# Kernel tuning notes

Hardware: AMD Instinct MI355X
Metric: run time of the kernel (lower is better)

The kernel has to match this reference:

```python
import jax, jax.numpy as jnp
import numpy as np

BZ, D_IN, D_STATE, D_OUT, L = 8, 256, 512, 256, 4096


def setup_inputs() -> dict:
    key = jax.random.key(0)
    k_u, k_a, k_b, k_c = jax.random.split(key, 4)
    init_scale = 0.5
    u = jax.random.normal(k_u, (BZ, D_IN, L), dtype=jnp.float32)
    A_unconstrained = jax.random.normal(k_a, (D_STATE,), dtype=jnp.float32) * 0.1
    B_mat = jax.random.normal(k_b, (D_STATE, D_IN), dtype=jnp.float32) * init_scale / np.sqrt(D_IN)
    C_mat = jax.random.normal(k_c, (D_OUT, D_STATE), dtype=jnp.float32) * init_scale / np.sqrt(D_STATE)
    D_mat = jnp.zeros((D_OUT, D_IN), dtype=jnp.float32)
    h0 = jnp.zeros((D_STATE,), dtype=jnp.float32)
    return {"u": u, "A_unconstrained": A_unconstrained, "B_mat": B_mat,
            "C_mat": C_mat, "D_mat": D_mat, "h0": h0}


def reference(u, A_unconstrained, B_mat, C_mat, D_mat, h0):
    # u: (B, input_dim, L)
    Bz = u.shape[0]
    A_diag = -jax.nn.softplus(A_unconstrained)          # (S,)
    # Precompute input projection for all timesteps: (L, B, S)
    Bu = jnp.einsum('bil,si->lbs', u, B_mat)
    state0 = jnp.broadcast_to(h0[None, :], (Bz, A_diag.shape[0]))

    def step(state, bu_t):
        x_t = state * A_diag[None, :] + bu_t            # (B, S)
        return x_t, x_t

    _, xs = jax.lax.scan(step, state0, Bu)              # xs: (L, B, S)
    # y_t = x_t @ C^T + u_t @ D^T, assembled as (B, output_dim, L)
    Y = jnp.einsum('lbs,os->bol', xs, C_mat) + jnp.einsum('bil,oi->bol', u, D_mat)
    return Y
```

## Files before the change

kernel.cpp:

```cpp
#include <hip/hip_runtime.h>
#include <math.h>

#define BZ 8
#define DI 256
#define DS 512
#define DOUT 256
#define LL 4096
#define BS (BZ * DS)
#define CH 64
#define CT 64

typedef __bf16 bf16x8 __attribute__((ext_vector_type(8)));
typedef float f32x4 __attribute__((ext_vector_type(4)));

__device__ __forceinline__ ushort f2b(float f) {
    union { float f; unsigned u; } v; v.f = f;
    unsigned r = v.u + 0x7FFFu + ((v.u >> 16) & 1u);
    return (ushort)(r >> 16);
}
__device__ __forceinline__ float b2f(ushort h) {
    union { unsigned u; float f; } v; v.u = ((unsigned)h) << 16;
    return v.f;
}

__device__ __forceinline__ void gload16(const ushort* g, ushort* l) {
    __builtin_amdgcn_global_load_lds(
        (const __attribute__((address_space(1))) unsigned int*)g,
        (__attribute__((address_space(3))) unsigned int*)l,
        16, 0, 0);
}

__global__ __launch_bounds__(256) void k_prep(const float* __restrict__ Au,
                                              float* __restrict__ apow,
                                              const float* __restrict__ Bm,
                                              const float* __restrict__ Cm,
                                              const float* __restrict__ Dm,
                                              ushort* __restrict__ Bmb,
                                              ushort* __restrict__ Cmb,
                                              ushort* __restrict__ Dmb) {
    const int t = blockIdx.x * 256 + threadIdx.x;
    const int n1 = DS * DI / 4, n2 = DOUT * DS / 4, n3 = DOUT * DI / 4;
    if (t < n1) {
        float4 v = ((const float4*)Bm)[t];
        ushort4 o; o.x = f2b(v.x); o.y = f2b(v.y); o.z = f2b(v.z); o.w = f2b(v.w);
        ((ushort4*)Bmb)[t] = o;
    } else if (t < n1 + n2) {
        float4 v = ((const float4*)Cm)[t - n1];
        ushort4 o; o.x = f2b(v.x); o.y = f2b(v.y); o.z = f2b(v.z); o.w = f2b(v.w);
        ((ushort4*)Cmb)[t - n1] = o;
    } else if (t < n1 + n2 + n3) {
        float4 v = ((const float4*)Dm)[t - n1 - n2];
        ushort4 o; o.x = f2b(v.x); o.y = f2b(v.y); o.z = f2b(v.z); o.w = f2b(v.w);
        ((ushort4*)Dmb)[t - n1 - n2] = o;
    }
    if (t < DS) {
        float x = Au[t];
        float sp = (x > 15.f) ? x : log1pf(expf(x));
        float ad = -sp;
        float p = 1.f;
        apow[t] = 1.f;
        for (int j = 1; j <= CT; ++j) { p *= ad; apow[j * DS + t] = p; }
    }
}

__global__ __launch_bounds__(256) void k_u2t(const float* __restrict__ u,
                                             ushort* __restrict__ utr) {
    __shared__ float T[64][65];
    const int tid = threadIdx.x;
    const int l0 = blockIdx.x * 64, i0 = blockIdx.y * 64, b = blockIdx.z;
    const int r = tid >> 4, c4 = tid & 15;
#pragma unroll
    for (int rr = r; rr < 64; rr += 16) {
        float4 v = *(const float4*)&u[((size_t)b * DI + i0 + rr) * LL + l0 + c4 * 4];
        T[rr][c4 * 4 + 0] = v.x; T[rr][c4 * 4 + 1] = v.y;
        T[rr][c4 * 4 + 2] = v.z; T[rr][c4 * 4 + 3] = v.w;
    }
    __syncthreads();
#pragma unroll
    for (int ll = r; ll < 64; ll += 16) {
        ushort4 o;
        o.x = f2b(T[c4 * 4 + 0][ll]); o.y = f2b(T[c4 * 4 + 1][ll]);
        o.z = f2b(T[c4 * 4 + 2][ll]); o.w = f2b(T[c4 * 4 + 3][ll]);
        *(ushort4*)&utr[((size_t)b * LL + l0 + ll) * DI + i0 + c4 * 4] = o;
    }
}

__global__ __launch_bounds__(256) void k_bu(const ushort* __restrict__ Bmb,
                                            const ushort* __restrict__ utr,
                                            ushort* __restrict__ Xb) {
    __shared__ ushort Abuf[128 * 32];
    __shared__ ushort Bbuf[128 * 32];
    const int tid = threadIdx.x;
    const int w = tid >> 6, lane = tid & 63;
    const int l0 = blockIdx.x * 128, s0 = blockIdx.y * 128, b = blockIdx.z;
    const int wm = w & 1, wn = w >> 1;
    const int mrow = lane & 15, quad = lane >> 4;
    const int sr = lane >> 2, sc = (lane & 3) * 8;

    f32x4 acc[4][4];
#pragma unroll
    for (int mi = 0; mi < 4; ++mi)
#pragma unroll
        for (int ni = 0; ni < 4; ++ni) acc[mi][ni] = (f32x4)0.f;

    const ushort* ag0 = Bmb + (size_t)(s0 + 16 * w + sr) * DI + sc;
    const ushort* ag1 = ag0 + (size_t)64 * DI;
    const ushort* bg0 = utr + ((size_t)b * LL + l0 + 16 * w + sr) * DI + sc;
    const ushort* bg1 = bg0 + (size_t)64 * DI;
    ushort* al0 = &Abuf[(16 * w) * 32];       ushort* al1 = &Abuf[(16 * w + 64) * 32];
    ushort* bl0 = &Bbuf[(16 * w) * 32];       ushort* bl1 = &Bbuf[(16 * w + 64) * 32];

    for (int kk = 0; kk < DI; kk += 32) {
        gload16(ag0 + kk, al0); gload16(ag1 + kk, al1);
        gload16(bg0 + kk, bl0); gload16(bg1 + kk, bl1);
        __syncthreads();
        bf16x8 af[4], bfr[4];
#pragma unroll
        for (int mi = 0; mi < 4; ++mi)
            af[mi] = *(const bf16x8*)&Abuf[(wm * 64 + mi * 16 + mrow) * 32 + quad * 8];
#pragma unroll
        for (int ni = 0; ni < 4; ++ni)
            bfr[ni] = *(const bf16x8*)&Bbuf[(wn * 64 + ni * 16 + mrow) * 32 + quad * 8];
#pragma unroll
        for (int mi = 0; mi < 4; ++mi)
#pragma unroll
            for (int ni = 0; ni < 4; ++ni)
                acc[mi][ni] = __builtin_amdgcn_mfma_f32_16x16x32_bf16(af[mi], bfr[ni], acc[mi][ni], 0, 0, 0);
        __syncthreads();
    }

#pragma unroll
    for (int mi = 0; mi < 4; ++mi) {
        const int s = s0 + wm * 64 + mi * 16 + quad * 4;
#pragma unroll
        for (int ni = 0; ni < 4; ++ni) {
            const int l = l0 + wn * 64 + ni * 16 + mrow;
            f32x4 v = acc[mi][ni];
            ushort4 o; o.x = f2b(v[0]); o.y = f2b(v[1]); o.z = f2b(v[2]); o.w = f2b(v[3]);
            *(ushort4*)&Xb[(size_t)l * BS + (size_t)b * DS + s] = o;
        }
    }
}

__global__ __launch_bounds__(256) void k_scan(ushort* __restrict__ Xb,
                                              float* __restrict__ finals,
                                              const float* __restrict__ apow) {
    const int c = blockIdx.x;
    const int bs = blockIdx.y * 256 + threadIdx.x;
    const int s = bs & (DS - 1);
    const float a = apow[DS + s];
    float acc = 0.f;
    ushort* p = Xb + (size_t)c * CT * BS + bs;
#pragma unroll 4
    for (int j = 0; j < CT; ++j) {
        acc = acc * a + b2f(*p);
        *p = f2b(acc);
        p += BS;
    }
    finals[(size_t)c * BS + bs] = acc;
}

__global__ __launch_bounds__(256) void k_carry(const float* __restrict__ finals,
                                               float* __restrict__ carries,
                                               const float* __restrict__ apow,
                                               const float* __restrict__ h0) {
    const int bs = blockIdx.x * 256 + threadIdx.x;
    const int s = bs & (DS - 1);
    const float aT = apow[CT * DS + s];
    float carry = h0[s];
    for (int c = 0; c < CH; ++c) {
        carries[(size_t)c * BS + bs] = carry;
        carry = aT * carry + finals[(size_t)c * BS + bs];
    }
}

__global__ __launch_bounds__(256) void k_correct(ushort* __restrict__ Xb,
                                                 const float* __restrict__ carries,
                                                 const float* __restrict__ apow) {
    const size_t i8 = (size_t)blockIdx.x * 256 + threadIdx.x;
    const size_t base = i8 * 8;
    const int t = (int)(base >> 12);
    const int bs0 = (int)(base & (BS - 1));
    const int c = t >> 6, j = t & (CT - 1);
    const int s0 = bs0 & (DS - 1);
    ushort4 xa = *(ushort4*)&Xb[base];
    ushort4 xb = *(ushort4*)&Xb[base + 4];
    float4 ca = *(const float4*)&carries[(size_t)c * BS + bs0];
    float4 cb = *(const float4*)&carries[(size_t)c * BS + bs0 + 4];
    const float* ap = &apow[(size_t)(j + 1) * DS + s0];
    float4 pa = *(const float4*)ap;
    float4 pb = *(const float4*)(ap + 4);
    ushort4 oa, ob;
    oa.x = f2b(b2f(xa.x) + pa.x * ca.x); oa.y = f2b(b2f(xa.y) + pa.y * ca.y);
    oa.z = f2b(b2f(xa.z) + pa.z * ca.z); oa.w = f2b(b2f(xa.w) + pa.w * ca.w);
    ob.x = f2b(b2f(xb.x) + pb.x * cb.x); ob.y = f2b(b2f(xb.y) + pb.y * cb.y);
    ob.z = f2b(b2f(xb.z) + pb.z * cb.z); ob.w = f2b(b2f(xb.w) + pb.w * cb.w);
    *(ushort4*)&Xb[base] = oa;
    *(ushort4*)&Xb[base + 4] = ob;
}

__global__ __launch_bounds__(256) void k_out(const ushort* __restrict__ Cmb,
                                             const ushort* __restrict__ Dmb,
                                             const ushort* __restrict__ Xb,
                                             const ushort* __restrict__ utr,
                                             float* __restrict__ Y) {
    __shared__ ushort Abuf[128 * 32];
    __shared__ ushort Bbuf[128 * 32];
    const int tid = threadIdx.x;
    const int w = tid >> 6, lane = tid & 63;
    const int l0 = blockIdx.x * 128, o0 = blockIdx.y * 128, b = blockIdx.z;
    const int wm = w & 1, wn = w >> 1;
    const int mrow = lane & 15, quad = lane >> 4;
    const int sr = lane >> 2, sc = (lane & 3) * 8;

    f32x4 acc[4][4];
#pragma unroll
    for (int mi = 0; mi < 4; ++mi)
#pragma unroll
        for (int ni = 0; ni < 4; ++ni) acc[mi][ni] = (f32x4)0.f;

    ushort* al0 = &Abuf[(16 * w) * 32];       ushort* al1 = &Abuf[(16 * w + 64) * 32];
    ushort* bl0 = &Bbuf[(16 * w) * 32];       ushort* bl1 = &Bbuf[(16 * w + 64) * 32];

    auto compute = [&]() {
        bf16x8 af[4], bfr[4];
#pragma unroll
        for (int mi = 0; mi < 4; ++mi)
            af[mi] = *(const bf16x8*)&Abuf[(wm * 64 + mi * 16 + mrow) * 32 + quad * 8];
#pragma unroll
        for (int ni = 0; ni < 4; ++ni)
            bfr[ni] = *(const bf16x8*)&Bbuf[(wn * 64 + ni * 16 + mrow) * 32 + quad * 8];
#pragma unroll
        for (int mi = 0; mi < 4; ++mi)
#pragma unroll
            for (int ni = 0; ni < 4; ++ni)
                acc[mi][ni] = __builtin_amdgcn_mfma_f32_16x16x32_bf16(af[mi], bfr[ni], acc[mi][ni], 0, 0, 0);
    };

    {
        const ushort* ag0 = Xb + (size_t)(l0 + 16 * w + sr) * BS + (size_t)b * DS + sc;
        const ushort* ag1 = ag0 + (size_t)64 * BS;
        const ushort* bg0 = Cmb + (size_t)(o0 + 16 * w + sr) * DS + sc;
        const ushort* bg1 = bg0 + (size_t)64 * DS;
        for (int kk = 0; kk < DS; kk += 32) {
            gload16(ag0 + kk, al0); gload16(ag1 + kk, al1);
            gload16(bg0 + kk, bl0); gload16(bg1 + kk, bl1);
            __syncthreads();
            compute();
            __syncthreads();
        }
    }
    {
        const ushort* ag0 = utr + ((size_t)b * LL + l0 + 16 * w + sr) * DI + sc;
        const ushort* ag1 = ag0 + (size_t)64 * DI;
        const ushort* bg0 = Dmb + (size_t)(o0 + 16 * w + sr) * DI + sc;
        const ushort* bg1 = bg0 + (size_t)64 * DI;
        for (int kk = 0; kk < DI; kk += 32) {
            gload16(ag0 + kk, al0); gload16(ag1 + kk, al1);
            gload16(bg0 + kk, bl0); gload16(bg1 + kk, bl1);
            __syncthreads();
            compute();
            __syncthreads();
        }
    }

#pragma unroll
    for (int mi = 0; mi < 4; ++mi) {
        const int l = l0 + wm * 64 + mi * 16 + quad * 4;
#pragma unroll
        for (int ni = 0; ni < 4; ++ni) {
            const int o = o0 + wn * 64 + ni * 16 + mrow;
            *(float4*)&Y[((size_t)b * DOUT + o) * LL + l] = *(float4*)&acc[mi][ni];
        }
    }
}

extern "C" void kernel_launch(void* const* d_in, const int* in_sizes, int n_in,
                              void* d_out, int out_size, void* d_ws, size_t ws_size,
                              hipStream_t stream) {
    const float* u  = (const float*)d_in[0];
    const float* Au = (const float*)d_in[1];
    const float* Bm = (const float*)d_in[2];
    const float* Cm = (const float*)d_in[3];
    const float* Dm = (const float*)d_in[4];
    const float* h0 = (const float*)d_in[5];
    float* Y = (float*)d_out;

    char* p = (char*)d_ws;
    ushort* utr    = (ushort*)p; p += (size_t)BZ * LL * DI * 2;
    ushort* Xb     = (ushort*)p; p += (size_t)LL * BS * 2;
    float* finals  = (float*)p;  p += (size_t)CH * BS * 4;
    float* carries = (float*)p;  p += (size_t)CH * BS * 4;
    float* apow    = (float*)p;  p += (size_t)(CT + 1) * DS * 4;
    ushort* Bmb    = (ushort*)p; p += (size_t)DS * DI * 2;
    ushort* Cmb    = (ushort*)p; p += (size_t)DOUT * DS * 2;
    ushort* Dmb    = (ushort*)p; p += (size_t)DOUT * DI * 2;

    k_prep<<<dim3(320), 256, 0, stream>>>(Au, apow, Bm, Cm, Dm, Bmb, Cmb, Dmb);
    k_u2t<<<dim3(LL / 64, DI / 64, BZ), 256, 0, stream>>>(u, utr);
    k_bu<<<dim3(LL / 128, DS / 128, BZ), 256, 0, stream>>>(Bmb, utr, Xb);
    k_scan<<<dim3(CH, BS / 256), 256, 0, stream>>>(Xb, finals, apow);
    k_carry<<<dim3(BS / 256), 256, 0, stream>>>(finals, carries, apow, h0);
    k_correct<<<dim3((int)(((size_t)LL * BS) / 8 / 256)), 256, 0, stream>>>(Xb, carries, apow);
    k_out<<<dim3(LL / 128, DOUT / 128, BZ), 256, 0, stream>>>(Cmb, Dmb, Xb, utr, Y);
}
```

Measured before the change: 168.7 us.

## Fuse chunk scan into Bu GEMM epilogue and carry correction into output GEMM

The per-chunk local scan now runs inside the k_bu epilogue on the tile staged in shared memory, which removes the separate k_scan pass over Xb. The carry correction is applied while loading the X tile in k_out, which removes the separate k_correct read-modify-write pass. Together these drop two full round trips of the large bf16 state buffer through global memory and two kernel launches. In exchange, k_out loads X through registers instead of async LDS loads, and k_bu gains a serial scan loop plus a larger padded shared-memory buffer that may lower occupancy.

Result: faster. 149.7 us (-11.2%).

```diff
diff --git a/kernel.cpp b/kernel.cpp
--- a/kernel.cpp
+++ b/kernel.cpp
@@ -9,9 +9,11 @@
 #define BS (BZ * DS)
 #define CH 64
 #define CT 64
+#define TST 136
 
 typedef __bf16 bf16x8 __attribute__((ext_vector_type(8)));
 typedef float f32x4 __attribute__((ext_vector_type(4)));
+typedef unsigned short us8 __attribute__((ext_vector_type(8)));
 
 __device__ __forceinline__ ushort f2b(float f) {
     union { float f; unsigned u; } v; v.f = f;
@@ -87,9 +89,12 @@
 
 __global__ __launch_bounds__(256) void k_bu(const ushort* __restrict__ Bmb,
                                             const ushort* __restrict__ utr,
-                                            ushort* __restrict__ Xb) {
-    __shared__ ushort Abuf[128 * 32];
-    __shared__ ushort Bbuf[128 * 32];
+                                            ushort* __restrict__ Xb,
+                                            float* __restrict__ finals,
+                                            const float* __restrict__ apow) {
+    __shared__ ushort smem[128 * TST];
+    ushort* Abuf = smem;
+    ushort* Bbuf = smem + 128 * 32;
     const int tid = threadIdx.x;
     const int w = tid >> 6, lane = tid & 63;
     const int l0 = blockIdx.x * 128, s0 = blockIdx.y * 128, b = blockIdx.z;
@@ -131,33 +136,39 @@
 
 #pragma unroll
     for (int mi = 0; mi < 4; ++mi) {
-        const int s = s0 + wm * 64 + mi * 16 + quad * 4;
+        const int sloc = wm * 64 + mi * 16 + quad * 4;
 #pragma unroll
         for (int ni = 0; ni < 4; ++ni) {
-            const int l = l0 + wn * 64 + ni * 16 + mrow;
+            const int lloc = wn * 64 + ni * 16 + mrow;
             f32x4 v = acc[mi][ni];
             ushort4 o; o.x = f2b(v[0]); o.y = f2b(v[1]); o.z = f2b(v[2]); o.w = f2b(v[3]);
-            *(ushort4*)&Xb[(size_t)l * BS + (size_t)b * DS + s] = o;
-        }
-    }
-}
-
-__global__ __launch_bounds__(256) void k_scan(ushort* __restrict__ Xb,
-                                              float* __restrict__ finals,
-                                              const float* __restrict__ apow) {
-    const int c = blockIdx.x;
-    const int bs = blockIdx.y * 256 + threadIdx.x;
-    const int s = bs & (DS - 1);
-    const float a = apow[DS + s];
-    float acc = 0.f;
-    ushort* p = Xb + (size_t)c * CT * BS + bs;
-#pragma unroll 4
-    for (int j = 0; j < CT; ++j) {
-        acc = acc * a + b2f(*p);
-        *p = f2b(acc);
-        p += BS;
-    }
-    finals[(size_t)c * BS + bs] = acc;
+            *(ushort4*)&smem[lloc * TST + sloc] = o;
+        }
+    }
+    __syncthreads();
+    {
+        const int cloc = tid >> 7, sl = tid & 127;
+        const float a = apow[DS + s0 + sl];
+        float acc2 = 0.f;
+        ushort* p = &smem[(cloc * 64) * TST + sl];
+#pragma unroll 8
+        for (int j = 0; j < CT; ++j) {
+            acc2 = a * acc2 + b2f(*p);
+            *p = f2b(acc2);
+            p += TST;
+        }
+        finals[(size_t)(l0 / 64 + cloc) * BS + (size_t)b * DS + s0 + sl] = acc2;
+    }
+    __syncthreads();
+    {
+        const int rr = tid >> 4, cc = tid & 15;
+#pragma unroll
+        for (int rep = 0; rep < 8; ++rep) {
+            const int l = rep * 16 + rr;
+            us8 v = *(const us8*)&smem[l * TST + cc * 8];
+            *(us8*)&Xb[(size_t)(l0 + l) * BS + (size_t)b * DS + s0 + cc * 8] = v;
+        }
+    }
 }
 
 __global__ __launch_bounds__(256) void k_carry(const float* __restrict__ finals,
@@ -174,37 +185,14 @@
     }
 }
 
-__global__ __launch_bounds__(256) void k_correct(ushort* __restrict__ Xb,
-                                                 const float* __restrict__ carries,
-                                                 const float* __restrict__ apow) {
-    const size_t i8 = (size_t)blockIdx.x * 256 + threadIdx.x;
-    const size_t base = i8 * 8;
-    const int t = (int)(base >> 12);
-    const int bs0 = (int)(base & (BS - 1));
-    const int c = t >> 6, j = t & (CT - 1);
-    const int s0 = bs0 & (DS - 1);
-    ushort4 xa = *(ushort4*)&Xb[base];
-    ushort4 xb = *(ushort4*)&Xb[base + 4];
-    float4 ca = *(const float4*)&carries[(size_t)c * BS + bs0];
-    float4 cb = *(const float4*)&carries[(size_t)c * BS + bs0 + 4];
-    const float* ap = &apow[(size_t)(j + 1) * DS + s0];
-    float4 pa = *(const float4*)ap;
-    float4 pb = *(const float4*)(ap + 4);
-    ushort4 oa, ob;
-    oa.x = f2b(b2f(xa.x) + pa.x * ca.x); oa.y = f2b(b2f(xa.y) + pa.y * ca.y);
-    oa.z = f2b(b2f(xa.z) + pa.z * ca.z); oa.w = f2b(b2f(xa.w) + pa.w * ca.w);
-    ob.x = f2b(b2f(xb.x) + pb.x * cb.x); ob.y = f2b(b2f(xb.y) + pb.y * cb.y);
-    ob.z = f2b(b2f(xb.z) + pb.z * cb.z); ob.w = f2b(b2f(xb.w) + pb.w * cb.w);
-    *(ushort4*)&Xb[base] = oa;
-    *(ushort4*)&Xb[base + 4] = ob;
-}
-
 __global__ __launch_bounds__(256) void k_out(const ushort* __restrict__ Cmb,
                                              const ushort* __restrict__ Dmb,
                                              const ushort* __restrict__ Xb,
                                              const ushort* __restrict__ utr,
+                                             const float* __restrict__ carries,
+                                             const float* __restrict__ apow,
                                              float* __restrict__ Y) {
-    __shared__ ushort Abuf[128 * 32];
+    __shared__ ushort Apad[128 * 40];
     __shared__ ushort Bbuf[128 * 32];
     const int tid = threadIdx.x;
     const int w = tid >> 6, lane = tid & 63;
@@ -219,14 +207,11 @@
 #pragma unroll
         for (int ni = 0; ni < 4; ++ni) acc[mi][ni] = (f32x4)0.f;
 
-    ushort* al0 = &Abuf[(16 * w) * 32];       ushort* al1 = &Abuf[(16 * w + 64) * 32];
-    ushort* bl0 = &Bbuf[(16 * w) * 32];       ushort* bl1 = &Bbuf[(16 * w + 64) * 32];
-
-    auto compute = [&]() {
+    auto compute = [&](const ushort* Ab, const int ast) {
         bf16x8 af[4], bfr[4];
 #pragma unroll
         for (int mi = 0; mi < 4; ++mi)
-            af[mi] = *(const bf16x8*)&Abuf[(wm * 64 + mi * 16 + mrow) * 32 + quad * 8];
+            af[mi] = *(const bf16x8*)&Ab[(wm * 64 + mi * 16 + mrow) * ast + quad * 8];
 #pragma unroll
         for (int ni = 0; ni < 4; ++ni)
             bfr[ni] = *(const bf16x8*)&Bbuf[(wn * 64 + ni * 16 + mrow) * 32 + quad * 8];
@@ -238,15 +223,47 @@
     };
 
     {
-        const ushort* ag0 = Xb + (size_t)(l0 + 16 * w + sr) * BS + (size_t)b * DS + sc;
-        const ushort* ag1 = ag0 + (size_t)64 * BS;
-        const ushort* bg0 = Cmb + (size_t)(o0 + 16 * w + sr) * DS + sc;
+        const int r0 = 16 * w + sr;
+        const int l_0 = l0 + r0, l_1 = l_0 + 64;
+        const int j0 = l_0 & 63, c0 = l_0 >> 6;
+        const int j1 = l_1 & 63, c1 = l_1 >> 6;
+        const float* ap0 = &apow[(size_t)(j0 + 1) * DS];
+        const float* ap1 = &apow[(size_t)(j1 + 1) * DS];
+        const float* cr0 = &carries[(size_t)c0 * BS + (size_t)b * DS];
+        const float* cr1 = &carries[(size_t)c1 * BS + (size_t)b * DS];
+        const ushort* x0 = Xb + (size_t)l_0 * BS + (size_t)b * DS;
+        const ushort* x1 = Xb + (size_t)l_1 * BS + (size_t)b * DS;
+        const ushort* bg0 = Cmb + (size_t)(o0 + r0) * DS + sc;
         const ushort* bg1 = bg0 + (size_t)64 * DS;
+        ushort* bl0 = &Bbuf[(16 * w) * 32];
+        ushort* bl1 = &Bbuf[(16 * w + 64) * 32];
         for (int kk = 0; kk < DS; kk += 32) {
-            gload16(ag0 + kk, al0); gload16(ag1 + kk, al1);
+            const int col = kk + sc;
             gload16(bg0 + kk, bl0); gload16(bg1 + kk, bl1);
+            {
+                us8 x = *(const us8*)&x0[col];
+                float4 pa = *(const float4*)&ap0[col], pb = *(const float4*)&ap0[col + 4];
+                float4 ca = *(const float4*)&cr0[col], cb = *(const float4*)&cr0[col + 4];
+                us8 o;
+                o[0] = f2b(b2f(x[0]) + pa.x * ca.x); o[1] = f2b(b2f(x[1]) + pa.y * ca.y);
+                o[2] = f2b(b2f(x[2]) + pa.z * ca.z); o[3] = f2b(b2f(x[3]) + pa.w * ca.w);
+                o[4] = f2b(b2f(x[4]) + pb.x * cb.x); o[5] = f2b(b2f(x[5]) + pb.y * cb.y);
+                o[6] = f2b(b2f(x[6]) + pb.z * cb.z); o[7] = f2b(b2f(x[7]) + pb.w * cb.w);
+                *(us8*)&Apad[r0 * 40 + sc] = o;
+            }
+            {
+                us8 x = *(const us8*)&x1[col];
+                float4 pa = *(const float4*)&ap1[col], pb = *(const float4*)&ap1[col + 4];
+                float4 ca = *(const float4*)&cr1[col], cb = *(const float4*)&cr1[col + 4];
+                us8 o;
+                o[0] = f2b(b2f(x[0]) + pa.x * ca.x); o[1] = f2b(b2f(x[1]) + pa.y * ca.y);
+                o[2] = f2b(b2f(x[2]) + pa.z * ca.z); o[3] = f2b(b2f(x[3]) + pa.w * ca.w);
+                o[4] = f2b(b2f(x[4]) + pb.x * cb.x); o[5] = f2b(b2f(x[5]) + pb.y * cb.y);
+                o[6] = f2b(b2f(x[6]) + pb.z * cb.z); o[7] = f2b(b2f(x[7]) + pb.w * cb.w);
+                *(us8*)&Apad[(r0 + 64) * 40 + sc] = o;
+            }
             __syncthreads();
-            compute();
+            compute(Apad, 40);
             __syncthreads();
         }
     }
@@ -255,11 +272,13 @@
         const ushort* ag1 = ag0 + (size_t)64 * DI;
         const ushort* bg0 = Dmb + (size_t)(o0 + 16 * w + sr) * DI + sc;
         const ushort* bg1 = bg0 + (size_t)64 * DI;
+        ushort* al0 = &Apad[(16 * w) * 32];       ushort* al1 = &Apad[(16 * w + 64) * 32];
+        ushort* bl0 = &Bbuf[(16 * w) * 32];       ushort* bl1 = &Bbuf[(16 * w + 64) * 32];
         for (int kk = 0; kk < DI; kk += 32) {
             gload16(ag0 + kk, al0); gload16(ag1 + kk, al1);
             gload16(bg0 + kk, bl0); gload16(bg1 + kk, bl1);
             __syncthreads();
-            compute();
+            compute(Apad, 32);
             __syncthreads();
         }
     }
@@ -298,9 +317,7 @@
 
     k_prep<<<dim3(320), 256, 0, stream>>>(Au, apow, Bm, Cm, Dm, Bmb, Cmb, Dmb);
     k_u2t<<<dim3(LL / 64, DI / 64, BZ), 256, 0, stream>>>(u, utr);
-    k_bu<<<dim3(LL / 128, DS / 128, BZ), 256, 0, stream>>>(Bmb, utr, Xb);
-    k_scan<<<dim3(CH, BS / 256), 256, 0, stream>>>(Xb, finals, apow);
+    k_bu<<<dim3(LL / 128, DS / 128, BZ), 256, 0, stream>>>(Bmb, utr, Xb, finals, apow);
     k_carry<<<dim3(BS / 256), 256, 0, stream>>>(finals, carries, apow, h0);
-    k_correct<<<dim3((int)(((size_t)LL * BS) / 8 / 256)), 256, 0, stream>>>(Xb, carries, apow);
-    k_out<<<dim3(LL / 128, DOUT / 128, BZ), 256, 0, stream>>>(Cmb, Dmb, Xb, utr, Y);
-}
+    k_out<<<dim3(LL / 128, DOUT / 128, BZ), 256, 0, stream>>>(Cmb, Dmb, Xb, utr, carries, apow, Y);
+}
```
